# Optimization experiments

Hardware: AMD Instinct MI355X
Metric: run time of the kernel (lower is better)

Reference implementation:

```python
import jax, jax.numpy as jnp
import numpy as np

BLOCK = 8      # block_size
NHEADS = 6     # num_heads
DIM = 192      # embed dim (C)


def setup_inputs() -> dict:
    key = jax.random.key(0)
    ks = jax.random.split(key, 5)
    B, C, H, W = 4, DIM, 256, 256
    x = jax.random.normal(ks[0], (B, C, H, W), dtype=jnp.float32)
    # torch nn.MultiheadAttention params: packed in-proj + out-proj (bias=True)
    in_proj_w = jax.random.normal(ks[1], (3 * C, C), dtype=jnp.float32) * 0.02
    in_proj_b = jnp.zeros((3 * C,), dtype=jnp.float32)
    out_proj_w = jax.random.normal(ks[2], (C, C), dtype=jnp.float32) * 0.02
    out_proj_b = jnp.zeros((C,), dtype=jnp.float32)
    return {"x": x, "in_proj_w": in_proj_w, "in_proj_b": in_proj_b,
            "out_proj_w": out_proj_w, "out_proj_b": out_proj_b}


def _block_attention(x, in_proj_w, in_proj_b, out_proj_w, out_proj_b):
    B, C, H, W = x.shape
    bs, nh = BLOCK, NHEADS
    hd = C // nh
    nH, nW = H // bs, W // bs
    S = bs * bs  # tokens per window
    # window partition: [B,C,H,W] -> [B*nH*nW, S, C]
    xw = x.reshape(B, C, nH, bs, nW, bs)
    xw = xw.transpose(0, 2, 4, 3, 5, 1).reshape(-1, S, C)
    N = xw.shape[0]
    # packed QKV projection (torch MultiheadAttention semantics)
    qkv = xw @ in_proj_w.T + in_proj_b              # [N,S,3C]
    q, k, v = jnp.split(qkv, 3, axis=-1)
    q = q.reshape(N, S, nh, hd) * (hd ** -0.5)
    k = k.reshape(N, S, nh, hd)
    v = v.reshape(N, S, nh, hd)
    scores = jnp.einsum('nqhd,nkhd->nhqk', q, k)    # [N,nh,S,S]
    attn = jax.nn.softmax(scores, axis=-1)
    out = jnp.einsum('nhqk,nkhd->nqhd', attn, v).reshape(N, S, C)
    out = out @ out_proj_w.T + out_proj_b           # [N,S,C]
    # inverse window permute: -> [B,C,H,W]
    out = out.reshape(B, nH, nW, bs, bs, C)
    out = out.transpose(0, 5, 1, 3, 2, 4).reshape(B, C, H, W)
    return out


def reference(x, in_proj_w, in_proj_b, out_proj_w, out_proj_b):
    return _block_attention(x, in_proj_w, in_proj_b, out_proj_w, out_proj_b)
```

## Files before the change

kernel.cpp:

```cpp
#include <hip/hip_runtime.h>
#include <hip/hip_bf16.h>

typedef __bf16 bf16;
typedef bf16  bf16x2 __attribute__((ext_vector_type(2)));
typedef bf16  bf16x4 __attribute__((ext_vector_type(4)));
typedef bf16  bf16x8 __attribute__((ext_vector_type(8)));
typedef float f32x4  __attribute__((ext_vector_type(4)));

#define DEVINL static __device__ __forceinline__

constexpr int C_ = 192, H_ = 256, W_ = 256;
constexpr int NWIN = 4096;
constexpr int THREADS = 384;
constexpr float QSCALE = 0.17677669529663687f;
constexpr float QS2    = 0.17677669529663687f * 1.4426950408889634f;

constexpr int K_BASE = 24576;
constexpr int V_BASE = 49152;
constexpr int LDS_BYTES = 73728;

constexpr int WQKV_N = 576 * 192;
constexpr int WOUT_N = 192 * 192;
constexpr size_t WS_NEED = (size_t)(WQKV_N + WOUT_N) * 2 + 576 * 4;

DEVINL char* xs_at(char* s, int row, int colbyte) {
    return s + ((row * 384 + colbyte) ^ ((row & 7) << 4));
}
DEVINL char* qk_at(char* s, int base, int row, int colbyte) {
    return s + base + ((row * 64 + colbyte) ^ (((row >> 2) & 3) << 4));
}
DEVINL char* vt_at(char* s, int h, int row, int colbyte) {
    return s + V_BASE + h * 4096 + ((row * 128 + colbyte) ^ ((row & 7) << 4));
}
DEVINL char* p_at(char* s, int h, int row, int colbyte) {
    const int base = (row & 32) ? (K_BASE + h * 4096) : (h * 4096);
    return s + base + (((row & 31) * 128 + colbyte) ^ ((row & 7) << 4));
}

DEVINL bf16x8 cvt8(const float* p) {
    float4 f0 = *(const float4*)p;
    float4 f1 = *(const float4*)(p + 4);
    bf16x8 r;
    r[0] = (bf16)f0.x; r[1] = (bf16)f0.y; r[2] = (bf16)f0.z; r[3] = (bf16)f0.w;
    r[4] = (bf16)f1.x; r[5] = (bf16)f1.y; r[6] = (bf16)f1.z; r[7] = (bf16)f1.w;
    return r;
}

template<int CTRL>
DEVINL float dppf(float x) {
    return __builtin_bit_cast(float, __builtin_amdgcn_update_dpp(
        0, __builtin_bit_cast(int, x), CTRL, 0xF, 0xF, true));
}
DEVINL float red_add16(float v) {
    v += dppf<0xB1>(v);
    v += dppf<0x4E>(v);
    v += dppf<0x141>(v);
    v += dppf<0x140>(v);
    return v;
}

__global__ void prep_weights(const float* __restrict__ wqkv, const float* __restrict__ bqkv,
                             const float* __restrict__ wout,
                             bf16* __restrict__ wq_f, bf16* __restrict__ wo_f,
                             float* __restrict__ bq_s) {
    int i = blockIdx.x * 256 + threadIdx.x;
    if (i < WQKV_N) {
        int e = i & 511, blk = i >> 9;
        int lane = e >> 3, j = e & 7;
        int g = lane >> 4, c = lane & 15;
        int ks = blk % 6, ct = (blk / 6) % 2, t = (blk / 12) % 3, hh = blk / 36;
        int col = t * 192 + 32 * hh + 16 * ct + c;
        int k = 32 * ks + 8 * g + j;
        float v = wqkv[col * 192 + k];
        if (t == 0) v *= QS2;
        wq_f[i] = (bf16)v;
    }
    int j2 = i - WQKV_N;
    if (j2 >= 0 && j2 < WOUT_N) {
        int e = j2 & 511, blk = j2 >> 9;
        int lane = e >> 3, jj = e & 7;
        int g = lane >> 4, c = lane & 15;
        int ks = blk % 6, cb = (blk / 6) % 2, hh = blk / 12;
        int col = 32 * hh + 16 * cb + c;
        int kpos = 32 * ks + 8 * g + jj;
        int kh = kpos >> 5, rem = kpos & 31, cc = rem >> 1, tt = rem & 1;
        int korig = (kh << 5) + 16 * tt + cc;
        wo_f[j2] = (bf16)wout[col * 192 + korig];
    }
    int k2 = i - (WQKV_N + WOUT_N);
    if (k2 >= 0 && k2 < 576) bq_s[k2] = bqkv[k2] * (k2 < 192 ? QS2 : 1.0f);
}

template<bool WB>
__global__ __launch_bounds__(THREADS, 4)
void block_attn(const float* __restrict__ x,
                const float* __restrict__ wqkv,
                const float* __restrict__ bqkv,
                const float* __restrict__ wout,
                const float* __restrict__ bout,
                const bf16*  __restrict__ wq_f,
                const bf16*  __restrict__ wo_f,
                const float* __restrict__ bq_s,
                float* __restrict__ out)
{
    extern __shared__ char smem[];

    const int tid  = threadIdx.x;
    const int lane = tid & 63;
    const int h    = tid >> 6;
    const int g    = lane >> 4;
    const int c    = lane & 15;

    const int win = (blockIdx.x & 7) * (NWIN / 8) + (blockIdx.x >> 3);
    const int b  = win >> 10;
    const int wh = (win >> 5) & 31;
    const int ww = win & 31;

    const size_t pixbase = ((size_t)b * C_) * (H_ * W_) + (size_t)(wh * 8) * W_ + ww * 8;
    const float* xwin = x   + pixbase;
    float*       owin = out + pixbase;

    auto ldw = [&](int t, int ct, int ks) -> bf16x8 {
        if (WB)
            return *(const bf16x8*)&wq_f[((((h*3 + t)*2 + ct)*6 + ks) << 9) + lane*8];
        const int col = t*192 + 32*h + 16*ct + c;
        return cvt8(wqkv + (size_t)col * C_ + 32*ks + 8*g);
    };

    #pragma unroll
    for (int hf = 0; hf < 2; ++hf) {
        float r[16];
        #pragma unroll
        for (int j = 0; j < 16; ++j)
            r[j] = xwin[(size_t)(32*h + 16*hf + j) * (H_ * W_) + (lane >> 3) * W_ + (lane & 7)];
        #pragma unroll
        for (int jj = 0; jj < 4; ++jj) {
            bf16x4 pk;
            pk[0] = (bf16)r[4*jj+0]; pk[1] = (bf16)r[4*jj+1];
            pk[2] = (bf16)r[4*jj+2]; pk[3] = (bf16)r[4*jj+3];
            *(bf16x4*)xs_at(smem, lane, 64*h + 32*hf + 8*jj) = pk;
        }
    }
    __syncthreads();

    {
        f32x4 acc[4][2];
        #pragma unroll
        for (int Mt = 0; Mt < 4; ++Mt)
            #pragma unroll
            for (int ct = 0; ct < 2; ++ct) acc[Mt][ct] = (f32x4){0.f, 0.f, 0.f, 0.f};

        bf16x8 wc0 = ldw(2, 0, 0), wc1 = ldw(2, 1, 0);
        #pragma unroll
        for (int ks = 0; ks < 6; ++ks) {
            bf16x8 a0 = *(const bf16x8*)xs_at(smem, 16*0 + c, 64*ks + 16*g);
            bf16x8 a1 = *(const bf16x8*)xs_at(smem, 16*1 + c, 64*ks + 16*g);
            bf16x8 a2 = *(const bf16x8*)xs_at(smem, 16*2 + c, 64*ks + 16*g);
            bf16x8 a3 = *(const bf16x8*)xs_at(smem, 16*3 + c, 64*ks + 16*g);
            bf16x8 wn0, wn1;
            if (ks < 5) { wn0 = ldw(2, 0, ks+1); wn1 = ldw(2, 1, ks+1); }
            __builtin_amdgcn_s_setprio(1);
            acc[0][0] = __builtin_amdgcn_mfma_f32_16x16x32_bf16(a0, wc0, acc[0][0], 0, 0, 0);
            acc[1][0] = __builtin_amdgcn_mfma_f32_16x16x32_bf16(a1, wc0, acc[1][0], 0, 0, 0);
            acc[2][0] = __builtin_amdgcn_mfma_f32_16x16x32_bf16(a2, wc0, acc[2][0], 0, 0, 0);
            acc[3][0] = __builtin_amdgcn_mfma_f32_16x16x32_bf16(a3, wc0, acc[3][0], 0, 0, 0);
            acc[0][1] = __builtin_amdgcn_mfma_f32_16x16x32_bf16(a0, wc1, acc[0][1], 0, 0, 0);
            acc[1][1] = __builtin_amdgcn_mfma_f32_16x16x32_bf16(a1, wc1, acc[1][1], 0, 0, 0);
            acc[2][1] = __builtin_amdgcn_mfma_f32_16x16x32_bf16(a2, wc1, acc[2][1], 0, 0, 0);
            acc[3][1] = __builtin_amdgcn_mfma_f32_16x16x32_bf16(a3, wc1, acc[3][1], 0, 0, 0);
            __builtin_amdgcn_s_setprio(0);
            wc0 = wn0; wc1 = wn1;
        }
        #pragma unroll
        for (int ct = 0; ct < 2; ++ct) {
            const float bias = (WB ? bq_s : bqkv)[384 + 32*h + 16*ct + c];
            #pragma unroll
            for (int r = 0; r < 4; ++r) {
                bf16x4 pk;
                pk[0] = (bf16)(acc[0][ct][r] + bias);
                pk[1] = (bf16)(acc[1][ct][r] + bias);
                pk[2] = (bf16)(acc[2][ct][r] + bias);
                pk[3] = (bf16)(acc[3][ct][r] + bias);
                *(bf16x4*)vt_at(smem, h, 16*ct + c, 32*g + 8*r) = pk;
            }
        }
    }

    {
        f32x4 acc[4][2];
        #pragma unroll
        for (int Mt = 0; Mt < 4; ++Mt)
            #pragma unroll
            for (int ct = 0; ct < 2; ++ct) acc[Mt][ct] = (f32x4){0.f, 0.f, 0.f, 0.f};

        bf16x8 wc0 = ldw(1, 0, 0), wc1 = ldw(1, 1, 0);
        #pragma unroll
        for (int ks = 0; ks < 6; ++ks) {
            bf16x8 a0 = *(const bf16x8*)xs_at(smem, 16*0 + c, 64*ks + 16*g);
            bf16x8 a1 = *(const bf16x8*)xs_at(smem, 16*1 + c, 64*ks + 16*g);
            bf16x8 a2 = *(const bf16x8*)xs_at(smem, 16*2 + c, 64*ks + 16*g);
            bf16x8 a3 = *(const bf16x8*)xs_at(smem, 16*3 + c, 64*ks + 16*g);
            bf16x8 wn0, wn1;
            if (ks < 5) { wn0 = ldw(1, 0, ks+1); wn1 = ldw(1, 1, ks+1); }
            __builtin_amdgcn_s_setprio(1);
            acc[0][0] = __builtin_amdgcn_mfma_f32_16x16x32_bf16(a0, wc0, acc[0][0], 0, 0, 0);
            acc[1][0] = __builtin_amdgcn_mfma_f32_16x16x32_bf16(a1, wc0, acc[1][0], 0, 0, 0);
            acc[2][0] = __builtin_amdgcn_mfma_f32_16x16x32_bf16(a2, wc0, acc[2][0], 0, 0, 0);
            acc[3][0] = __builtin_amdgcn_mfma_f32_16x16x32_bf16(a3, wc0, acc[3][0], 0, 0, 0);
            acc[0][1] = __builtin_amdgcn_mfma_f32_16x16x32_bf16(a0, wc1, acc[0][1], 0, 0, 0);
            acc[1][1] = __builtin_amdgcn_mfma_f32_16x16x32_bf16(a1, wc1, acc[1][1], 0, 0, 0);
            acc[2][1] = __builtin_amdgcn_mfma_f32_16x16x32_bf16(a2, wc1, acc[2][1], 0, 0, 0);
            acc[3][1] = __builtin_amdgcn_mfma_f32_16x16x32_bf16(a3, wc1, acc[3][1], 0, 0, 0);
            __builtin_amdgcn_s_setprio(0);
            wc0 = wn0; wc1 = wn1;
        }
        const float b0 = (WB ? bq_s : bqkv)[192 + 32*h + c];
        const float b1 = (WB ? bq_s : bqkv)[192 + 32*h + 16 + c];
        #pragma unroll
        for (int Mt = 0; Mt < 4; ++Mt)
            #pragma unroll
            for (int r = 0; r < 4; ++r) {
                bf16x2 pk2;
                pk2[0] = (bf16)(acc[Mt][0][r] + b0);
                pk2[1] = (bf16)(acc[Mt][1][r] + b1);
                *(bf16x2*)qk_at(smem, K_BASE + h*4096, 16*Mt + 4*g + r, 4*c) = pk2;
            }
    }

    {
        f32x4 acc[4][2];
        #pragma unroll
        for (int Mt = 0; Mt < 4; ++Mt)
            #pragma unroll
            for (int ct = 0; ct < 2; ++ct) acc[Mt][ct] = (f32x4){0.f, 0.f, 0.f, 0.f};

        bf16x8 wc0 = ldw(0, 0, 0), wc1 = ldw(0, 1, 0);
        #pragma unroll
        for (int ks = 0; ks < 6; ++ks) {
            bf16x8 a0 = *(const bf16x8*)xs_at(smem, 16*0 + c, 64*ks + 16*g);
            bf16x8 a1 = *(const bf16x8*)xs_at(smem, 16*1 + c, 64*ks + 16*g);
            bf16x8 a2 = *(const bf16x8*)xs_at(smem, 16*2 + c, 64*ks + 16*g);
            bf16x8 a3 = *(const bf16x8*)xs_at(smem, 16*3 + c, 64*ks + 16*g);
            bf16x8 wn0, wn1;
            if (ks < 5) { wn0 = ldw(0, 0, ks+1); wn1 = ldw(0, 1, ks+1); }
            __builtin_amdgcn_s_setprio(1);
            acc[0][0] = __builtin_amdgcn_mfma_f32_16x16x32_bf16(a0, wc0, acc[0][0], 0, 0, 0);
            acc[1][0] = __builtin_amdgcn_mfma_f32_16x16x32_bf16(a1, wc0, acc[1][0], 0, 0, 0);
            acc[2][0] = __builtin_amdgcn_mfma_f32_16x16x32_bf16(a2, wc0, acc[2][0], 0, 0, 0);
            acc[3][0] = __builtin_amdgcn_mfma_f32_16x16x32_bf16(a3, wc0, acc[3][0], 0, 0, 0);
            acc[0][1] = __builtin_amdgcn_mfma_f32_16x16x32_bf16(a0, wc1, acc[0][1], 0, 0, 0);
            acc[1][1] = __builtin_amdgcn_mfma_f32_16x16x32_bf16(a1, wc1, acc[1][1], 0, 0, 0);
            acc[2][1] = __builtin_amdgcn_mfma_f32_16x16x32_bf16(a2, wc1, acc[2][1], 0, 0, 0);
            acc[3][1] = __builtin_amdgcn_mfma_f32_16x16x32_bf16(a3, wc1, acc[3][1], 0, 0, 0);
            __builtin_amdgcn_s_setprio(0);
            wc0 = wn0; wc1 = wn1;
        }
        __syncthreads();

        const float b0 = (WB ? bq_s : bqkv)[32*h + c];
        const float b1 = (WB ? bq_s : bqkv)[32*h + 16 + c];
        #pragma unroll
        for (int Mt = 0; Mt < 4; ++Mt)
            #pragma unroll
            for (int r = 0; r < 4; ++r) {
                float q0 = acc[Mt][0][r] + b0, q1 = acc[Mt][1][r] + b1;
                if (!WB) { q0 *= QS2; q1 *= QS2; }
                bf16x2 pq; pq[0] = (bf16)q0; pq[1] = (bf16)q1;
                *(bf16x2*)qk_at(smem, h*4096, 16*Mt + 4*g + r, 4*c) = pq;
            }
    }

    {
        bf16x8 kb[4], qa[4];
        #pragma unroll
        for (int kMt = 0; kMt < 4; ++kMt)
            kb[kMt] = *(const bf16x8*)qk_at(smem, K_BASE + h * 4096, 16*kMt + c, 16*g);
        #pragma unroll
        for (int qMt = 0; qMt < 4; ++qMt)
            qa[qMt] = *(const bf16x8*)qk_at(smem, h * 4096, 16*qMt + c, 16*g);
        const f32x4 zf = (f32x4){0.f, 0.f, 0.f, 0.f};

        #pragma unroll
        for (int qp = 0; qp < 2; ++qp) {
            f32x4 sc[2][4];
            __builtin_amdgcn_s_setprio(1);
            #pragma unroll
            for (int kMt = 0; kMt < 4; ++kMt)
                #pragma unroll
                for (int i = 0; i < 2; ++i)
                    sc[i][kMt] = __builtin_amdgcn_mfma_f32_16x16x32_bf16(qa[2*qp + i], kb[kMt], zf, 0, 0, 0);
            __builtin_amdgcn_s_setprio(0);
            #pragma unroll
            for (int i = 0; i < 2; ++i) {
                #pragma unroll
                for (int r = 0; r < 4; ++r) {
                    float e0 = exp2f(sc[i][0][r]);
                    float e1 = exp2f(sc[i][1][r]);
                    float e2 = exp2f(sc[i][2][r]);
                    float e3 = exp2f(sc[i][3][r]);
                    float s = red_add16(e0 + e1 + e2 + e3);
                    float inv = 1.0f / s;
                    sc[i][0][r] = e0 * inv; sc[i][1][r] = e1 * inv;
                    sc[i][2][r] = e2 * inv; sc[i][3][r] = e3 * inv;
                }
            }
            #pragma unroll
            for (int i = 0; i < 2; ++i)
                #pragma unroll
                for (int r = 0; r < 4; ++r) {
                    bf16x4 pp;
                    pp[0] = (bf16)sc[i][0][r]; pp[1] = (bf16)sc[i][1][r];
                    pp[2] = (bf16)sc[i][2][r]; pp[3] = (bf16)sc[i][3][r];
                    *(bf16x4*)p_at(smem, h, 16*(2*qp + i) + 4*g + r, 8*c) = pp;
                }
        }
    }

    f32x4 oacc[4][2];
    #pragma unroll
    for (int qMt = 0; qMt < 4; ++qMt)
        #pragma unroll
        for (int ct2 = 0; ct2 < 2; ++ct2) oacc[qMt][ct2] = (f32x4){0.f, 0.f, 0.f, 0.f};

    #pragma unroll
    for (int ks2 = 0; ks2 < 2; ++ks2) {
        bf16x8 pa[4];
        #pragma unroll
        for (int qMt = 0; qMt < 4; ++qMt)
            pa[qMt] = *(const bf16x8*)p_at(smem, h, 16*qMt + c, 64*ks2 + 16*g);
        __builtin_amdgcn_s_setprio(1);
        #pragma unroll
        for (int ct2 = 0; ct2 < 2; ++ct2) {
            bf16x8 vb = *(const bf16x8*)vt_at(smem, h, 16*ct2 + c, 64*ks2 + 16*g);
            #pragma unroll
            for (int qMt = 0; qMt < 4; ++qMt)
                oacc[qMt][ct2] = __builtin_amdgcn_mfma_f32_16x16x32_bf16(pa[qMt], vb, oacc[qMt][ct2], 0, 0, 0);
        }
        __builtin_amdgcn_s_setprio(0);
    }
    #pragma unroll
    for (int qMt = 0; qMt < 4; ++qMt)
        #pragma unroll
        for (int r = 0; r < 4; ++r) {
            const int row = 16*qMt + 4*g + r;
            if (WB) {
                bf16x2 pa2;
                pa2[0] = (bf16)oacc[qMt][0][r];
                pa2[1] = (bf16)oacc[qMt][1][r];
                *(bf16x2*)p_at(smem, h, row, 4*c) = pa2;
            } else {
                *(bf16*)p_at(smem, h, row, 2*c)        = (bf16)oacc[qMt][0][r];
                *(bf16*)p_at(smem, h, row, 32 + 2*c)   = (bf16)oacc[qMt][1][r];
            }
        }
    __syncthreads();

    f32x4 oo[2][4];
    #pragma unroll
    for (int cb = 0; cb < 2; ++cb)
        #pragma unroll
        for (int m = 0; m < 4; ++m) oo[cb][m] = (f32x4){0.f, 0.f, 0.f, 0.f};

    {
        auto ldo = [&](int cb, int ks) -> bf16x8 {
            if (WB)
                return *(const bf16x8*)&wo_f[(((h*2 + cb)*6 + ks) << 9) + lane*8];
            return cvt8(wout + (size_t)(32*h + 16*cb + c) * C_ + 32*ks + 8*g);
        };
        bf16x8 wc0 = ldo(0, 0), wc1 = ldo(1, 0);
        #pragma unroll
        for (int ks = 0; ks < 6; ++ks) {
            bf16x8 wn0, wn1;
            if (ks < 5) { wn0 = ldo(0, ks+1); wn1 = ldo(1, ks+1); }
            __builtin_amdgcn_s_setprio(1);
            #pragma unroll
            for (int m = 0; m < 4; ++m) {
                bf16x8 at = *(const bf16x8*)p_at(smem, ks, 16*m + c, 16*g);
                oo[0][m] = __builtin_amdgcn_mfma_f32_16x16x32_bf16(wc0, at, oo[0][m], 0, 0, 0);
                oo[1][m] = __builtin_amdgcn_mfma_f32_16x16x32_bf16(wc1, at, oo[1][m], 0, 0, 0);
            }
            __builtin_amdgcn_s_setprio(0);
            wc0 = wn0; wc1 = wn1;
        }
    }
    #pragma unroll
    for (int cb = 0; cb < 2; ++cb) {
        float bo[4];
        #pragma unroll
        for (int r = 0; r < 4; ++r) bo[r] = bout[32*h + 16*cb + 4*g + r];
        #pragma unroll
        for (int m = 0; m < 4; ++m)
            #pragma unroll
            for (int r = 0; r < 4; ++r)
                owin[(size_t)(32*h + 16*cb + 4*g + r) * (H_ * W_)
                     + (size_t)(2*m + (c >> 3)) * W_ + (c & 7)] = oo[cb][m][r] + bo[r];
    }
}

extern "C" void kernel_launch(void* const* d_in, const int* in_sizes, int n_in,
                              void* d_out, int out_size, void* d_ws, size_t ws_size,
                              hipStream_t stream) {
    const float* x    = (const float*)d_in[0];
    const float* wqkv = (const float*)d_in[1];
    const float* bqkv = (const float*)d_in[2];
    const float* wout = (const float*)d_in[3];
    const float* bout = (const float*)d_in[4];
    float* out = (float*)d_out;

    bf16*  wq_f = (bf16*)d_ws;
    bf16*  wo_f = wq_f + WQKV_N;
    float* bq_s = (float*)(wo_f + WOUT_N);

    const bool wb = (ws_size >= WS_NEED) && (d_ws != nullptr);

    if (wb) {
        hipFuncSetAttribute((const void*)block_attn<true>,
                            hipFuncAttributeMaxDynamicSharedMemorySize, LDS_BYTES);
        prep_weights<<<(WQKV_N + WOUT_N + 576 + 255) / 256, 256, 0, stream>>>(
            wqkv, bqkv, wout, wq_f, wo_f, bq_s);
        block_attn<true><<<NWIN, THREADS, LDS_BYTES, stream>>>(
            x, wqkv, bqkv, wout, bout, wq_f, wo_f, bq_s, out);
    } else {
        hipFuncSetAttribute((const void*)block_attn<false>,
                            hipFuncAttributeMaxDynamicSharedMemorySize, LDS_BYTES);
        block_attn<false><<<NWIN, THREADS, LDS_BYTES, stream>>>(
            x, wqkv, bqkv, wout, bout, wq_f, wo_f, bq_s, out);
    }
}
```

Baseline: 208.3 us.

## Keep V projection in registers as MFMA B operand, drop V LDS staging

The V projection output is packed straight from the MFMA accumulators into bf16x8 B-operand registers, so V no longer takes a round trip through LDS. The softmax probabilities are written with a permuted key order so the P·V reduction index matches the register layout of V. LDS drops from 72 KB to 48 KB per block, which could allow more resident blocks per CU, and the input load is merged into one 32-element pass. In exchange, register pressure rises from holding V and the larger load array, and the P stores become narrower two-element writes.

```diff
diff --git a/kernel.cpp b/kernel.cpp
--- a/kernel.cpp
+++ b/kernel.cpp
@@ -12,12 +12,10 @@
 constexpr int C_ = 192, H_ = 256, W_ = 256;
 constexpr int NWIN = 4096;
 constexpr int THREADS = 384;
-constexpr float QSCALE = 0.17677669529663687f;
-constexpr float QS2    = 0.17677669529663687f * 1.4426950408889634f;
+constexpr float QS2 = 0.17677669529663687f * 1.4426950408889634f;
 
 constexpr int K_BASE = 24576;
-constexpr int V_BASE = 49152;
-constexpr int LDS_BYTES = 73728;
+constexpr int LDS_BYTES = 49152;
 
 constexpr int WQKV_N = 576 * 192;
 constexpr int WOUT_N = 192 * 192;
@@ -28,9 +26,6 @@
 }
 DEVINL char* qk_at(char* s, int base, int row, int colbyte) {
     return s + base + ((row * 64 + colbyte) ^ (((row >> 2) & 3) << 4));
-}
-DEVINL char* vt_at(char* s, int h, int row, int colbyte) {
-    return s + V_BASE + h * 4096 + ((row * 128 + colbyte) ^ ((row & 7) << 4));
 }
 DEVINL char* p_at(char* s, int h, int row, int colbyte) {
     const int base = (row & 32) ? (K_BASE + h * 4096) : (h * 4096);
@@ -127,21 +122,22 @@
         return cvt8(wqkv + (size_t)col * C_ + 32*ks + 8*g);
     };
 
-    #pragma unroll
-    for (int hf = 0; hf < 2; ++hf) {
-        float r[16];
-        #pragma unroll
-        for (int j = 0; j < 16; ++j)
-            r[j] = xwin[(size_t)(32*h + 16*hf + j) * (H_ * W_) + (lane >> 3) * W_ + (lane & 7)];
-        #pragma unroll
-        for (int jj = 0; jj < 4; ++jj) {
+    {
+        float r[32];
+        #pragma unroll
+        for (int j = 0; j < 32; ++j)
+            r[j] = xwin[(size_t)(32 * h + j) * (H_ * W_) + (lane >> 3) * W_ + (lane & 7)];
+        #pragma unroll
+        for (int jj = 0; jj < 8; ++jj) {
             bf16x4 pk;
             pk[0] = (bf16)r[4*jj+0]; pk[1] = (bf16)r[4*jj+1];
             pk[2] = (bf16)r[4*jj+2]; pk[3] = (bf16)r[4*jj+3];
-            *(bf16x4*)xs_at(smem, lane, 64*h + 32*hf + 8*jj) = pk;
+            *(bf16x4*)xs_at(smem, lane, 64 * h + 8 * jj) = pk;
         }
     }
     __syncthreads();
+
+    bf16x8 vb[2][2];
 
     {
         f32x4 acc[4][2];
@@ -175,13 +171,14 @@
         for (int ct = 0; ct < 2; ++ct) {
             const float bias = (WB ? bq_s : bqkv)[384 + 32*h + 16*ct + c];
             #pragma unroll
-            for (int r = 0; r < 4; ++r) {
-                bf16x4 pk;
-                pk[0] = (bf16)(acc[0][ct][r] + bias);
-                pk[1] = (bf16)(acc[1][ct][r] + bias);
-                pk[2] = (bf16)(acc[2][ct][r] + bias);
-                pk[3] = (bf16)(acc[3][ct][r] + bias);
-                *(bf16x4*)vt_at(smem, h, 16*ct + c, 32*g + 8*r) = pk;
+            for (int ks2 = 0; ks2 < 2; ++ks2) {
+                bf16x8 f;
+                #pragma unroll
+                for (int r = 0; r < 4; ++r) {
+                    f[2*r+0] = (bf16)(acc[2*ks2+0][ct][r] + bias);
+                    f[2*r+1] = (bf16)(acc[2*ks2+1][ct][r] + bias);
+                }
+                vb[ct][ks2] = f;
             }
         }
     }
@@ -279,6 +276,7 @@
         for (int qMt = 0; qMt < 4; ++qMt)
             qa[qMt] = *(const bf16x8*)qk_at(smem, h * 4096, 16*qMt + c, 16*g);
         const f32x4 zf = (f32x4){0.f, 0.f, 0.f, 0.f};
+        const int K0 = 8 * (c >> 2) + 2 * (c & 3);
 
         #pragma unroll
         for (int qp = 0; qp < 2; ++qp) {
@@ -308,10 +306,12 @@
             for (int i = 0; i < 2; ++i)
                 #pragma unroll
                 for (int r = 0; r < 4; ++r) {
-                    bf16x4 pp;
-                    pp[0] = (bf16)sc[i][0][r]; pp[1] = (bf16)sc[i][1][r];
-                    pp[2] = (bf16)sc[i][2][r]; pp[3] = (bf16)sc[i][3][r];
-                    *(bf16x4*)p_at(smem, h, 16*(2*qp + i) + 4*g + r, 8*c) = pp;
+                    const int row = 16*(2*qp + i) + 4*g + r;
+                    bf16x2 w0, w1;
+                    w0[0] = (bf16)sc[i][0][r]; w0[1] = (bf16)sc[i][1][r];
+                    w1[0] = (bf16)sc[i][2][r]; w1[1] = (bf16)sc[i][3][r];
+                    *(bf16x2*)p_at(smem, h, row, 2*K0)        = w0;
+                    *(bf16x2*)p_at(smem, h, row, 2*(32 + K0)) = w1;
                 }
         }
     }
@@ -330,12 +330,10 @@
             pa[qMt] = *(const bf16x8*)p_at(smem, h, 16*qMt + c, 64*ks2 + 16*g);
         __builtin_amdgcn_s_setprio(1);
         #pragma unroll
-        for (int ct2 = 0; ct2 < 2; ++ct2) {
-            bf16x8 vb = *(const bf16x8*)vt_at(smem, h, 16*ct2 + c, 64*ks2 + 16*g);
+        for (int ct2 = 0; ct2 < 2; ++ct2)
             #pragma unroll
             for (int qMt = 0; qMt < 4; ++qMt)
-                oacc[qMt][ct2] = __builtin_amdgcn_mfma_f32_16x16x32_bf16(pa[qMt], vb, oacc[qMt][ct2], 0, 0, 0);
-        }
+                oacc[qMt][ct2] = __builtin_amdgcn_mfma_f32_16x16x32_bf16(pa[qMt], vb[ct2][ks2], oacc[qMt][ct2], 0, 0, 0);
         __builtin_amdgcn_s_setprio(0);
     }
     #pragma unroll
```

Result: slower. 223.5 us (+7.3%).
